# Performance work log

Measured on AMD Instinct MI355X. Metric: run time of the kernel, lower is better.

Reference implementation:

```python
import jax, jax.numpy as jnp
import numpy as np

B, T, D, H = 2, 2048, 768, 12
HS = D // H


def setup_inputs() -> dict:
    key = jax.random.key(0)
    ks = jax.random.split(key, 11)
    s = 1.0 / np.sqrt(D)
    return {
        "query": jax.random.normal(ks[0], (B, T, D), jnp.float32),
        "key": jax.random.normal(ks[1], (B, T, D), jnp.float32),
        "value": jax.random.normal(ks[2], (B, T, D), jnp.float32),
        "Wq": jax.random.normal(ks[3], (D, D), jnp.float32) * s,
        "bq": jax.random.normal(ks[4], (D,), jnp.float32) * s,
        "Wk": jax.random.normal(ks[5], (D, D), jnp.float32) * s,
        "bk": jax.random.normal(ks[6], (D,), jnp.float32) * s,
        "Wv": jax.random.normal(ks[7], (D, D), jnp.float32) * s,
        "bv": jax.random.normal(ks[8], (D,), jnp.float32) * s,
        "Wo": jax.random.normal(ks[9], (D, D), jnp.float32) * s,
        "bo": jax.random.normal(ks[10], (D,), jnp.float32) * s,
    }


def reference(query, key, value, Wq, bq, Wk, bk, Wv, bv, Wo, bo):
    # Projections (torch nn.Linear: x @ W.T + b), then split heads -> [B,H,T,HS]
    def split_heads(x):
        return x.reshape(B, -1, H, HS).transpose(0, 2, 1, 3)

    q = split_heads(query @ Wq.T + bq)
    k = split_heads(key @ Wk.T + bk)
    v = split_heads(value @ Wv.T + bv)

    scale = 1.0 / jnp.sqrt(jnp.asarray(HS, q.dtype))
    scores = jnp.einsum("bhqd,bhkd->bhqk", q, k) * scale  # [B,H,Tq,Tk]
    attn = jax.nn.softmax(scores, axis=-1)
    out = jnp.einsum("bhqk,bhkd->bhqd", attn, v)  # [B,H,Tq,HS]
    out = out.transpose(0, 2, 1, 3).reshape(B, -1, D)
    output = out @ Wo.T + bo
    return output, attn.mean(axis=1)
```

## Files before the change

### kernel.cpp

```cpp
#include <hip/hip_runtime.h>
#include <hip/hip_fp16.h>
#include <stdint.h>

typedef _Float16 f16;
typedef _Float16 f16x8 __attribute__((ext_vector_type(8)));
typedef _Float16 f16x4v __attribute__((ext_vector_type(4)));
typedef __fp16 h16x2 __attribute__((ext_vector_type(2)));
typedef float f32x4 __attribute__((ext_vector_type(4)));
typedef float f32x16 __attribute__((ext_vector_type(16)));

#define MFMA32(a,b,c) __builtin_amdgcn_mfma_f32_32x32x16_f16(a,b,c,0,0,0)
#define CVTPK(a,b) __builtin_amdgcn_cvt_pkrtz(a,b)

#if __has_builtin(__builtin_amdgcn_exp2f)
#define EXP2(x) __builtin_amdgcn_exp2f(x)
#else
#define EXP2(x) exp2f(x)
#endif

static __device__ __forceinline__ float dot2acc(h16x2 a, float c) {
#if __has_builtin(__builtin_amdgcn_fdot2)
    const h16x2 one = { (__fp16)1.f, (__fp16)1.f };
    return __builtin_amdgcn_fdot2(a, one, c, false);
#else
    return c + (float)a[0] + (float)a[1];
#endif
}

typedef __attribute__((address_space(1))) void gvoid_t;
typedef __attribute__((address_space(3))) void svoid_t;
#define AS1(p) ((gvoid_t*)(uintptr_t)(p))
#define AS3(p) ((svoid_t*)(uint32_t)(uintptr_t)(p))

static constexpr int Bc = 2, Tc = 2048, Dc = 768, Hc = 12;
static constexpr int Mc = Bc * Tc;
static constexpr float SC2 = 0.18033688011112042f;

union PA { f16x8 v; h16x2 h[4]; };

#define FKEY(R) ((((R) & 7)) ^ (((R) >> 3) & 3))

#define FRAG32(BASE, ROWOFF, CHUNK) \
    (*(const f16x8*)((const char*)(BASE) + \
        ((ROWOFF) + q32) * 128 + (((CHUNK) ^ FKEY(q32)) * 16)))

#define FRAGP(BASE, ROWOFF, C) \
    (*(const f16x8*)((const char*)(BASE) + \
        (((ROWOFF) / 2 + (q32 >> 1)) * 128) + \
        (((((q32 & 1) << 2) | (C)) ^ FKEY((ROWOFF) / 2 + (q32 >> 1))) * 16)))

__global__ __launch_bounds__(256) void conv_all(
    const float* __restrict__ q, const float* __restrict__ k, const float* __restrict__ v,
    const float* __restrict__ wq, const float* __restrict__ wk, const float* __restrict__ wv,
    const float* __restrict__ wo,
    f16* __restrict__ qh, f16* __restrict__ kh, f16* __restrict__ vh,
    f16* __restrict__ wqh, f16* __restrict__ wkh, f16* __restrict__ wvh, f16* __restrict__ woh)
{
    const int NI = (Mc * Dc) / 4;
    const int NW = (Dc * Dc) / 4;
    int i = blockIdx.x * 256 + threadIdx.x;
    if (i >= 3 * NI + 4 * NW) return;
    const float4* src; f16* dst; int j; float scl = 1.f;
    if (i < 3 * NI) {
        int a = i / NI; j = i - a * NI;
        src = (const float4*)(a == 0 ? q : (a == 1 ? k : v));
        dst = (a == 0 ? qh : (a == 1 ? kh : vh));
    } else {
        int t = i - 3 * NI;
        int a = t / NW; j = t - a * NW;
        src = (const float4*)(a == 0 ? wq : (a == 1 ? wk : (a == 2 ? wv : wo)));
        dst = (a == 0 ? wqh : (a == 1 ? wkh : (a == 2 ? wvh : woh)));
        if (a == 0) scl = SC2;
    }
    float4 f = src[j];
    f16x4v o = { (f16)(f.x * scl), (f16)(f.y * scl), (f16)(f.z * scl), (f16)(f.w * scl) };
    *(f16x4v*)(dst + 4 * j) = o;
}

__device__ __forceinline__ void gemm_bk32(
    const f16* __restrict__ A, const f16* __restrict__ W,
    int brow, int bcol, char* As, char* Bs, f32x16 acc[2])
{
    const int tid = threadIdx.x;
    const int w = tid >> 6, lane = tid & 63;
    const int q32 = lane & 31, hi = lane >> 5;
    const int wr = w >> 1, wc = w & 1;
    const int wbase16 = (tid & ~63) * 16;

#define GSA(KT_, BUF_) do { \
    const int k0_ = (KT_) * 32; \
    _Pragma("unroll") \
    for (int j_ = 0; j_ < 2; ++j_) { \
        const int p_ = j_ * 256 + tid; \
        const int L_ = p_ >> 3, c8_ = (p_ & 7) ^ FKEY(L_); \
        const int row_ = 2 * L_ + (c8_ >> 2), kc_ = (c8_ & 3) * 8; \
        __builtin_amdgcn_global_load_lds(AS1(A + (size_t)(brow + row_) * 768 + k0_ + kc_), \
            AS3(As + (BUF_) * 8192 + j_ * 4096 + wbase16), 16, 0, 0); \
    } } while (0)
#define GSB(KT_, BUF_) do { \
    const int k0_ = (KT_) * 32; \
    const int L_ = tid >> 3, c8_ = (tid & 7) ^ FKEY(L_); \
    const int row_ = 2 * L_ + (c8_ >> 2), kc_ = (c8_ & 3) * 8; \
    __builtin_amdgcn_global_load_lds(AS1(W + (size_t)(bcol + row_) * 768 + k0_ + kc_), \
        AS3(Bs + (BUF_) * 4096 + wbase16), 16, 0, 0); \
    } while (0)

    GSA(0, 0); GSB(0, 0);
    __syncthreads();
    for (int kt = 0; kt < 24; ++kt) {
        const int cur = kt & 1;
        if (kt < 23) { GSA(kt + 1, cur ^ 1); GSB(kt + 1, cur ^ 1); }
        const char* As_ = As + cur * 8192;
        const char* Bs_ = Bs + cur * 4096;
#pragma unroll
        for (int ks = 0; ks < 2; ++ks) {
            const f16x8 af0 = FRAGP(As_, wr * 64,      ks * 2 + hi);
            const f16x8 af1 = FRAGP(As_, wr * 64 + 32, ks * 2 + hi);
            const f16x8 bf  = FRAGP(Bs_, wc * 32,      ks * 2 + hi);
            acc[0] = MFMA32(af0, bf, acc[0]);
            acc[1] = MFMA32(af1, bf, acc[1]);
        }
        __syncthreads();
    }
#undef GSA
#undef GSB
}

__global__ __launch_bounds__(256) void qkv_proj(
    const f16* __restrict__ qh, const f16* __restrict__ kh, const f16* __restrict__ vh,
    const f16* __restrict__ wqh, const f16* __restrict__ wkh, const f16* __restrict__ wvh,
    const float* __restrict__ bq, const float* __restrict__ bk, const float* __restrict__ bv,
    f16* __restrict__ Qp, f16* __restrict__ Kp, f16* __restrict__ Vt)
{
    __shared__ char lds[24576];
    char* As = lds; char* Bs = lds + 16384;

    const int z = blockIdx.z;
    const f16* A = (z == 0) ? qh : (z == 1) ? kh : vh;
    const f16* W = (z == 0) ? wqh : (z == 1) ? wkh : wvh;
    const float* bias = (z == 0) ? bq : (z == 1) ? bk : bv;
    const int brow = blockIdx.y * 128, bcol = blockIdx.x * 64;

    f32x16 acc[2];
#pragma unroll
    for (int mi = 0; mi < 2; ++mi)
#pragma unroll
        for (int r = 0; r < 16; ++r) acc[mi][r] = 0.f;

    gemm_bk32(A, W, brow, bcol, As, Bs, acc);

    const int tid = threadIdx.x, w = tid >> 6, lane = tid & 63;
    const int q32 = lane & 31, hi = lane >> 5;
    const int wr = w >> 1, wc = w & 1;
    const int c = bcol + wc * 32 + q32;
    const float bval = (z == 0) ? bias[c] * SC2 : bias[c];

    if (z < 2) {
        f16* dst = (z == 0) ? Qp : Kp;
#pragma unroll
        for (int mi = 0; mi < 2; ++mi)
#pragma unroll
            for (int r = 0; r < 16; ++r) {
                const int row = brow + wr * 64 + mi * 32 + (r & 3) + 8 * (r >> 2) + 4 * hi;
                dst[(size_t)row * 768 + c] = (f16)(acc[mi][r] + bval);
            }
    } else {
        __syncthreads();
        const int dl = wc * 32 + q32;
#pragma unroll
        for (int mi = 0; mi < 2; ++mi)
#pragma unroll
            for (int j = 0; j < 8; ++j) {
                const int r0 = 2 * j;
                const int crow = (r0 & 3) + 8 * (r0 >> 2) + 4 * hi;
                const int sw = ((crow >> 2) ^ (crow >> 3)) & 1;
                const int tp = crow ^ (sw * 12);
                const int tloc = wr * 64 + mi * 32 + tp;
                const h16x2 pv = CVTPK(acc[mi][r0] + bval, acc[mi][r0 + 1] + bval);
                *(h16x2*)(As + dl * 256 + ((tloc * 2) ^ ((dl & 7) << 4))) = pv;
            }
        __syncthreads();
        const int bb = brow >> 11, t0 = brow & 2047, hh = bcol >> 6;
        f16* Vh = Vt + ((size_t)(bb * 12 + hh) * 64) * 2048;
#pragma unroll
        for (int j = 0; j < 4; ++j) {
            const int dr = j * 16 + (tid >> 4), off = tid & 15;
            const f16x8 vv = *(const f16x8*)(As + dr * 256 + ((off * 16) ^ ((dr & 7) << 4)));
            *(f16x8*)(Vh + (size_t)dr * 2048 + t0 + off * 8) = vv;
        }
    }
}

__global__ __launch_bounds__(256, 4) void attn_out(
    const f16* __restrict__ Qp, const f16* __restrict__ Kp, const f16* __restrict__ Vt,
    float* __restrict__ l_inv, f16* __restrict__ ctx)
{
    __shared__ char arena[33280];

    f16* Kbuf0 = (f16*)(arena);
    f16* Kbuf1 = (f16*)(arena + 8192);
    f16* Vbuf0 = (f16*)(arena + 16384);
    f16* Vbuf1 = (f16*)(arena + 24576);
    float (*Ored)[32][64] = (float (*)[32][64])(arena);
    float (*lred)[2][32]  = (float (*)[2][32])(arena + 16384);

    const int qt = blockIdx.x, h = blockIdx.y, b = blockIdx.z;
    const int tid = threadIdx.x, w = tid >> 6, lane = tid & 63;
    const int q32 = lane & 31, hi = lane >> 5;
    const int qh = w & 1, kh = w >> 1;
    const int wbase16 = (tid & ~63) * 16;

    const size_t qrow0 = (size_t)b * 2048 + qt * 64 + qh * 32;
    const int hcol = h * 64;

    const f16* qb = Qp + (qrow0 + q32) * 768 + hcol + hi * 8;
    f16x8 bqf[4];
#pragma unroll
    for (int d = 0; d < 4; ++d) bqf[d] = *(const f16x8*)(qb + d * 16);

    const size_t kbase = (size_t)b * 2048;
    const f16* Vg = Vt + ((size_t)(b * 12 + h)) * 64 * 2048;

    f32x16 oacc[2];
#pragma unroll
    for (int dt = 0; dt < 2; ++dt)
#pragma unroll
        for (int r = 0; r < 16; ++r) oacc[dt][r] = 0.f;
    float lsum = 0.f;

#define STAGE_KV(KT_, KB_, VB_) do { \
    _Pragma("unroll") \
    for (int j_ = 0; j_ < 2; ++j_) { \
        const int p_ = j_ * 256 + tid; \
        const int row_ = p_ >> 3, c_ = (p_ & 7) ^ FKEY(row_); \
        __builtin_amdgcn_global_load_lds( \
            AS1(Kp + (kbase + (size_t)(KT_) * 64 + row_) * 768 + hcol + c_ * 8), \
            AS3((char*)(KB_) + j_ * 4096 + wbase16), 16, 0, 0); \
        __builtin_amdgcn_global_load_lds( \
            AS1(Vg + (size_t)row_ * 2048 + (KT_) * 64 + c_ * 8), \
            AS3((char*)(VB_) + j_ * 4096 + wbase16), 16, 0, 0); \
    } } while (0)

#define AOBODY(KB_, VB_) do { \
    const f16* Kb_ = (KB_); const f16* Vb_ = (VB_); \
    f32x16 sa; \
    _Pragma("unroll") \
    for (int r_ = 0; r_ < 16; ++r_) sa[r_] = 0.f; \
    sa = MFMA32(FRAG32(Kb_, kh * 32, 0 + hi), bqf[0], sa); \
    sa = MFMA32(FRAG32(Kb_, kh * 32, 2 + hi), bqf[1], sa); \
    sa = MFMA32(FRAG32(Kb_, kh * 32, 4 + hi), bqf[2], sa); \
    sa = MFMA32(FRAG32(Kb_, kh * 32, 6 + hi), bqf[3], sa); \
    float p[16]; \
    _Pragma("unroll") \
    for (int r_ = 0; r_ < 16; ++r_) p[r_] = EXP2(sa[r_]); \
    PA pa0, pa1; \
    pa0.h[0] = CVTPK(p[0], p[1]);   pa0.h[1] = CVTPK(p[2], p[3]); \
    pa0.h[2] = CVTPK(p[4], p[5]);   pa0.h[3] = CVTPK(p[6], p[7]); \
    pa1.h[0] = CVTPK(p[8], p[9]);   pa1.h[1] = CVTPK(p[10], p[11]); \
    pa1.h[2] = CVTPK(p[12], p[13]); pa1.h[3] = CVTPK(p[14], p[15]); \
    float t0_ = 0.f, t1_ = 0.f; \
    t0_ = dot2acc(pa0.h[0], t0_); t0_ = dot2acc(pa0.h[1], t0_); \
    t0_ = dot2acc(pa0.h[2], t0_); t0_ = dot2acc(pa0.h[3], t0_); \
    t1_ = dot2acc(pa1.h[0], t1_); t1_ = dot2acc(pa1.h[1], t1_); \
    t1_ = dot2acc(pa1.h[2], t1_); t1_ = dot2acc(pa1.h[3], t1_); \
    lsum += t0_ + t1_; \
    oacc[0] = MFMA32(FRAG32(Vb_, 0,  kh * 4 + 0 + hi), pa0.v, oacc[0]); \
    oacc[0] = MFMA32(FRAG32(Vb_, 0,  kh * 4 + 2 + hi), pa1.v, oacc[0]); \
    oacc[1] = MFMA32(FRAG32(Vb_, 32, kh * 4 + 0 + hi), pa0.v, oacc[1]); \
    oacc[1] = MFMA32(FRAG32(Vb_, 32, kh * 4 + 2 + hi), pa1.v, oacc[1]); \
} while (0)

    STAGE_KV(0, Kbuf0, Vbuf0);
    __syncthreads();
    for (int kt = 0; kt < 32; kt += 2) {
        STAGE_KV(kt + 1, Kbuf1, Vbuf1);
        AOBODY(Kbuf0, Vbuf0);
        __syncthreads();
        if (kt < 30) STAGE_KV(kt + 2, Kbuf0, Vbuf0);
        AOBODY(Kbuf1, Vbuf1);
        __syncthreads();
    }
#undef STAGE_KV
#undef AOBODY

    lsum += __shfl_xor(lsum, 32);
    if (hi == 0) lred[kh][qh][q32] = lsum;
    if (kh == 1) {
#pragma unroll
        for (int dt = 0; dt < 2; ++dt)
#pragma unroll
            for (int g = 0; g < 4; ++g) {
                float4 v4 = { oacc[dt][g * 4 + 0], oacc[dt][g * 4 + 1],
                              oacc[dt][g * 4 + 2], oacc[dt][g * 4 + 3] };
                *(float4*)&Ored[qh][q32][dt * 32 + g * 8 + hi * 4] = v4;
            }
    }
    __syncthreads();
    if (kh == 0) {
        const float iv = 1.f / (lred[0][qh][q32] + lred[1][qh][q32]);
        if (hi == 0)
            l_inv[((size_t)(b * 12 + h)) * 2048 + qt * 64 + qh * 32 + q32] = iv;
        f16* cb = ctx + (qrow0 + q32) * 768 + hcol;
#pragma unroll
        for (int dt = 0; dt < 2; ++dt)
#pragma unroll
            for (int g = 0; g < 4; ++g) {
                const int d0 = dt * 32 + g * 8 + hi * 4;
                const float4 o4 = *(const float4*)&Ored[qh][q32][d0];
                f16x4v s;
#pragma unroll
                for (int e = 0; e < 4; ++e)
                    s[e] = (f16)((oacc[dt][g * 4 + e] + (&o4.x)[e]) * iv);
                *(f16x4v*)(cb + d0) = s;
            }
    }
}

__global__ __launch_bounds__(256) void tail_fused(
    const f16* __restrict__ ctx, const f16* __restrict__ woh,
    const float* __restrict__ bo, float* __restrict__ out,
    const f16* __restrict__ Qp, const f16* __restrict__ Kp,
    const float* __restrict__ l_inv, float* __restrict__ om)
{
    __shared__ char sh[32768];

    const int tid = threadIdx.x, w = tid >> 6, lane = tid & 63;
    const int q32 = lane & 31, hi = lane >> 5;
    const int wbase16 = (tid & ~63) * 16;

    if (blockIdx.x < 384) {
        const int brow = (blockIdx.x / 12) * 128, bcol = (blockIdx.x % 12) * 64;
        f32x16 acc[2];
#pragma unroll
        for (int mi = 0; mi < 2; ++mi)
#pragma unroll
            for (int r = 0; r < 16; ++r) acc[mi][r] = 0.f;

        gemm_bk32(ctx, woh, brow, bcol, sh, sh + 16384, acc);

        const int wr = w >> 1, wc = w & 1;
        const int c = bcol + wc * 32 + q32;
        const float bval = bo[c];
#pragma unroll
        for (int mi = 0; mi < 2; ++mi)
#pragma unroll
            for (int r = 0; r < 16; ++r) {
                const int row = brow + wr * 64 + mi * 32 + (r & 3) + 8 * (r >> 2) + 4 * hi;
                out[(size_t)row * 768 + c] = acc[mi][r] + bval;
            }
    } else {
        const int mb = blockIdx.x - 384;
        const int kt = mb & 31, r2 = mb >> 5;
        const int qt = r2 & 31, b = r2 >> 5;
        const int qh = w & 1, kh = w >> 1;

        char* Qb = sh;
        char* Kb = sh + 16384;

        const size_t qtrow = (size_t)b * 2048 + qt * 64;
        const size_t ktrow = (size_t)b * 2048 + kt * 64;

        f32x16 macc;
#pragma unroll
        for (int r = 0; r < 16; ++r) macc[r] = 0.f;

#define MSTAGE(H_, BUF) do { \
    _Pragma("unroll") \
    for (int j_ = 0; j_ < 2; ++j_) { \
        const int p_ = j_ * 256 + tid; \
        const int row_ = p_ >> 3, c_ = (p_ & 7) ^ FKEY(row_); \
        __builtin_amdgcn_global_load_lds( \
            AS1(Qp + (qtrow + row_) * 768 + (H_) * 64 + c_ * 8), \
            AS3(Qb + (BUF) * 8192 + j_ * 4096 + wbase16), 16, 0, 0); \
        __builtin_amdgcn_global_load_lds( \
            AS1(Kp + (ktrow + row_) * 768 + (H_) * 64 + c_ * 8), \
            AS3(Kb + (BUF) * 8192 + j_ * 4096 + wbase16), 16, 0, 0); \
    } } while (0)

#define MBODY(H_, CUR) do { \
    const f16* Qb_ = (const f16*)(Qb + (CUR) * 8192); \
    const f16* Kb_ = (const f16*)(Kb + (CUR) * 8192); \
    f16x8 qf[4]; \
    _Pragma("unroll") \
    for (int d_ = 0; d_ < 4; ++d_) qf[d_] = FRAG32(Qb_, qh * 32, d_ * 2 + hi); \
    f32x16 sa; \
    _Pragma("unroll") \
    for (int r_ = 0; r_ < 16; ++r_) sa[r_] = 0.f; \
    sa = MFMA32(FRAG32(Kb_, kh * 32, 0 + hi), qf[0], sa); \
    sa = MFMA32(FRAG32(Kb_, kh * 32, 2 + hi), qf[1], sa); \
    sa = MFMA32(FRAG32(Kb_, kh * 32, 4 + hi), qf[2], sa); \
    sa = MFMA32(FRAG32(Kb_, kh * 32, 6 + hi), qf[3], sa); \
    const float ivv = l_inv[((size_t)(b * 12 + (H_))) * 2048 + qt * 64 + qh * 32 + q32]; \
    _Pragma("unroll") \
    for (int r_ = 0; r_ < 16; ++r_) macc[r_] += EXP2(sa[r_]) * ivv; \
} while (0)

        MSTAGE(0, 0);
        __syncthreads();
        for (int h = 0; h < 12; ++h) {
            const int cur = h & 1;
            if (h < 11) MSTAGE(h + 1, cur ^ 1);
            MBODY(h, cur);
            __syncthreads();
        }
#undef MSTAGE
#undef MBODY

        float* ob = om + ((size_t)(b * 2048 + qt * 64 + qh * 32 + q32)) * 2048
                  + kt * 64 + kh * 32;
#pragma unroll
        for (int g = 0; g < 4; ++g) {
            float4 v4 = { macc[g * 4 + 0] * (1.0f / 12.0f),
                          macc[g * 4 + 1] * (1.0f / 12.0f),
                          macc[g * 4 + 2] * (1.0f / 12.0f),
                          macc[g * 4 + 3] * (1.0f / 12.0f) };
            *(float4*)(ob + g * 8 + hi * 4) = v4;
        }
    }
}

extern "C" void kernel_launch(void* const* d_in, const int* in_sizes, int n_in,
                              void* d_out, int out_size, void* d_ws, size_t ws_size,
                              hipStream_t stream) {
    const float* q  = (const float*)d_in[0];
    const float* k  = (const float*)d_in[1];
    const float* v  = (const float*)d_in[2];
    const float* Wq = (const float*)d_in[3];
    const float* bq = (const float*)d_in[4];
    const float* Wk = (const float*)d_in[5];
    const float* bk = (const float*)d_in[6];
    const float* Wv = (const float*)d_in[7];
    const float* bv = (const float*)d_in[8];
    const float* Wo = (const float*)d_in[9];
    const float* bo = (const float*)d_in[10];
    float* out = (float*)d_out;

    char* ws = (char*)d_ws;
    const size_t SZ_IN = (size_t)Mc * Dc * 2;
    const size_t SZ_W  = (size_t)Dc * Dc * 2;
    f16* qh  = (f16*)(ws);
    f16* kh  = (f16*)(ws + SZ_IN);
    f16* vh  = (f16*)(ws + 2 * SZ_IN);
    f16* wqh = (f16*)(ws + 3 * SZ_IN);
    f16* wkh = (f16*)(ws + 3 * SZ_IN + SZ_W);
    f16* wvh = (f16*)(ws + 3 * SZ_IN + 2 * SZ_W);
    f16* woh = (f16*)(ws + 3 * SZ_IN + 3 * SZ_W);
    f16* Qp  = (f16*)(ws + 3 * SZ_IN + 4 * SZ_W);
    f16* Kp  = (f16*)(ws + 4 * SZ_IN + 4 * SZ_W);
    f16* Vt  = (f16*)(ws + 5 * SZ_IN + 4 * SZ_W);
    f16* ctx = qh;
    float* l_inv = (float*)kh;

    conv_all<<<dim3(11520), dim3(256), 0, stream>>>(q, k, v, Wq, Wk, Wv, Wo,
                                                    qh, kh, vh, wqh, wkh, wvh, woh);
    qkv_proj<<<dim3(12, 32, 3), dim3(256), 0, stream>>>(qh, kh, vh, wqh, wkh, wvh,
                                                        bq, bk, bv, Qp, Kp, Vt);
    attn_out<<<dim3(32, 12, 2), dim3(256), 0, stream>>>(Qp, Kp, Vt, l_inv, ctx);
    tail_fused<<<dim3(2432), dim3(256), 0, stream>>>(ctx, woh, bo, out,
                                                     Qp, Kp, l_inv,
                                                     out + (size_t)Mc * Dc);
}
```

Baseline: 130.0 us.

## Deepen attn-mean pipeline to 4 LDS stages with explicit vmcnt waits

The attention-mean branch of the tail kernel now uses a 4-slot LDS ring with prefetch distance 2 instead of double buffering. It uses manual s_waitcnt vmcnt counts plus a single s_barrier per head instead of __syncthreads after each body. The 12 l_inv loads are hoisted into registers up front, and the head loop is fully unrolled. This aims to hide global-to-LDS latency, at the cost of doubling shared memory to 64KB, which may lower occupancy, and of relying on hand-counted waitcnts.

```diff
diff --git a/kernel.cpp b/kernel.cpp
--- a/kernel.cpp
+++ b/kernel.cpp
@@ -322,7 +322,7 @@
     const f16* __restrict__ Qp, const f16* __restrict__ Kp,
     const float* __restrict__ l_inv, float* __restrict__ om)
 {
-    __shared__ char sh[32768];
+    __shared__ char sh[65536];
 
     const int tid = threadIdx.x, w = tid >> 6, lane = tid & 63;
     const int q32 = lane & 31, hi = lane >> 5;
@@ -354,32 +354,34 @@
         const int qt = r2 & 31, b = r2 >> 5;
         const int qh = w & 1, kh = w >> 1;
 
-        char* Qb = sh;
-        char* Kb = sh + 16384;
-
         const size_t qtrow = (size_t)b * 2048 + qt * 64;
         const size_t ktrow = (size_t)b * 2048 + kt * 64;
 
+        float ivv[12];
+#pragma unroll
+        for (int h = 0; h < 12; ++h)
+            ivv[h] = l_inv[((size_t)(b * 12 + h)) * 2048 + qt * 64 + qh * 32 + q32];
+
         f32x16 macc;
 #pragma unroll
         for (int r = 0; r < 16; ++r) macc[r] = 0.f;
 
-#define MSTAGE(H_, BUF) do { \
+#define MSTAGE(H_, S_) do { \
     _Pragma("unroll") \
     for (int j_ = 0; j_ < 2; ++j_) { \
         const int p_ = j_ * 256 + tid; \
         const int row_ = p_ >> 3, c_ = (p_ & 7) ^ FKEY(row_); \
         __builtin_amdgcn_global_load_lds( \
             AS1(Qp + (qtrow + row_) * 768 + (H_) * 64 + c_ * 8), \
-            AS3(Qb + (BUF) * 8192 + j_ * 4096 + wbase16), 16, 0, 0); \
+            AS3(sh + (S_) * 16384 + j_ * 4096 + wbase16), 16, 0, 0); \
         __builtin_amdgcn_global_load_lds( \
             AS1(Kp + (ktrow + row_) * 768 + (H_) * 64 + c_ * 8), \
-            AS3(Kb + (BUF) * 8192 + j_ * 4096 + wbase16), 16, 0, 0); \
+            AS3(sh + (S_) * 16384 + 8192 + j_ * 4096 + wbase16), 16, 0, 0); \
     } } while (0)
 
-#define MBODY(H_, CUR) do { \
-    const f16* Qb_ = (const f16*)(Qb + (CUR) * 8192); \
-    const f16* Kb_ = (const f16*)(Kb + (CUR) * 8192); \
+#define MBODY(H_, S_) do { \
+    const f16* Qb_ = (const f16*)(sh + (S_) * 16384); \
+    const f16* Kb_ = (const f16*)(sh + (S_) * 16384 + 8192); \
     f16x8 qf[4]; \
     _Pragma("unroll") \
     for (int d_ = 0; d_ < 4; ++d_) qf[d_] = FRAG32(Qb_, qh * 32, d_ * 2 + hi); \
@@ -390,18 +392,25 @@
     sa = MFMA32(FRAG32(Kb_, kh * 32, 2 + hi), qf[1], sa); \
     sa = MFMA32(FRAG32(Kb_, kh * 32, 4 + hi), qf[2], sa); \
     sa = MFMA32(FRAG32(Kb_, kh * 32, 6 + hi), qf[3], sa); \
-    const float ivv = l_inv[((size_t)(b * 12 + (H_))) * 2048 + qt * 64 + qh * 32 + q32]; \
-    _Pragma("unroll") \
-    for (int r_ = 0; r_ < 16; ++r_) macc[r_] += EXP2(sa[r_]) * ivv; \
+    const float iv_ = ivv[H_]; \
+    _Pragma("unroll") \
+    for (int r_ = 0; r_ < 16; ++r_) macc[r_] += EXP2(sa[r_]) * iv_; \
 } while (0)
 
         MSTAGE(0, 0);
-        __syncthreads();
+        MSTAGE(1, 1);
+        asm volatile("s_waitcnt vmcnt(4) lgkmcnt(0)" ::: "memory");
+        __builtin_amdgcn_sched_barrier(0);
+        __builtin_amdgcn_s_barrier();
+#pragma unroll
         for (int h = 0; h < 12; ++h) {
-            const int cur = h & 1;
-            if (h < 11) MSTAGE(h + 1, cur ^ 1);
-            MBODY(h, cur);
-            __syncthreads();
+            if (h + 2 < 12) MSTAGE(h + 2, (h + 2) & 3);
+            if (h <= 9)       asm volatile("s_waitcnt vmcnt(8) lgkmcnt(0)" ::: "memory");
+            else if (h == 10) asm volatile("s_waitcnt vmcnt(4) lgkmcnt(0)" ::: "memory");
+            else              asm volatile("s_waitcnt vmcnt(0) lgkmcnt(0)" ::: "memory");
+            __builtin_amdgcn_sched_barrier(0);
+            __builtin_amdgcn_s_barrier();
+            MBODY(h, h & 3);
         }
 #undef MSTAGE
 #undef MBODY
```

New measurement: 135.7 us. 4.4% more time.
